# Performance work log

Hardware: AMD Instinct MI355X
Metric: run time of the kernel (lower is better)

## Reference

```python
import jax, jax.numpy as jnp
import numpy as np

N_NODES = 50000
N_EDGES = 800000
D = 64
D_OUT = 64


def setup_inputs() -> dict:
    key = jax.random.key(0)
    ks = jax.random.split(key, 7)
    h_src = jax.random.normal(ks[0], (N_NODES, D), dtype=jnp.float32)
    h_dst = jax.random.normal(ks[1], (N_NODES, D), dtype=jnp.float32)
    e = jax.random.normal(ks[2], (N_EDGES, D), dtype=jnp.float32)
    src = jax.random.randint(ks[3], (N_EDGES,), 0, N_NODES, dtype=jnp.int32)
    dst = jax.random.randint(ks[4], (N_EDGES,), 0, N_NODES, dtype=jnp.int32)
    W = jax.random.normal(ks[5], (D_OUT, 2 * D), dtype=jnp.float32) * 0.05  # nn.Linear weight [out, in]
    b = jax.random.normal(ks[6], (D_OUT,), dtype=jnp.float32) * 0.05
    return {"h_src": h_src, "h_dst": h_dst, "e": e, "src": src, "dst": dst, "W": W, "b": b}


def reference(h_src, h_dst, e, src, dst, W, b):
    # u_dot_e: per-edge dot product between gathered src features and edge features
    h_u = h_src[src]                                   # [E, D] gather
    score = jnp.sum(h_u * e, axis=-1)                  # [E]
    exp_s = jnp.exp(score)                             # raw exp, as in original (no max-subtract)
    # segment-sum exp over dst nodes, then edge-wise normalize (edge softmax)
    denom = jax.ops.segment_sum(exp_s, dst, num_segments=N_NODES)  # [N]
    pi = exp_s / denom[dst]                            # [E]
    # weighted neighbor aggregation: sum_e pi * h_src[src] into dst
    msg = h_u * pi[:, None]                            # [E, D]
    h_sum = jax.ops.segment_sum(msg, dst, num_segments=N_NODES)    # [N, D]
    # concat self features with aggregated neighbors, then linear
    h_total = jnp.concatenate([h_dst, h_sum], axis=1)  # [N, 2D]
    return h_total @ W.T + b                           # [N, D_OUT]
```

## Files before the change

### kernel.cpp

```cpp
#include <hip/hip_runtime.h>

#define N_NODES 50000
#define N_EDGES 800000
#define D 64
#define CAP 64

typedef float vf4 __attribute__((ext_vector_type(4)));

__global__ __launch_bounds__(256) void k1_bucket(
    const int* __restrict__ src, const int* __restrict__ dst,
    int* __restrict__ count, int2* __restrict__ slots) {
    int i = blockIdx.x * 256 + threadIdx.x;
    int s = src[i];
    int d = dst[i];
    int pos = atomicAdd(&count[d], 1);
    if (pos < CAP)
        slots[(size_t)d * CAP + pos] = make_int2(s, i);
}

__global__ __launch_bounds__(256, 4) void k2_agg(
    const vf4* __restrict__ h_src4, const vf4* __restrict__ e4,
    const int* __restrict__ count, const int2* __restrict__ slots,
    vf4* __restrict__ h_sum4) {
    int t = threadIdx.x;
    int node = blockIdx.x * 16 + (t >> 4);
    int l16 = t & 15;
    int cnt = count[node];
    cnt = cnt < CAP ? cnt : CAP;
    const int2* row = slots + (size_t)node * CAP;
    vf4 acc = {0.f, 0.f, 0.f, 0.f};
    float dsum = 0.f;
    int2 se = make_int2(0, 0);
    if (l16 < 8 && l16 < cnt) se = row[l16];
    for (int base = 0; base < cnt; base += 8) {
        int2 se_cur = se;
        int nxt = base + 8;
        se = make_int2(0, 0);
        if (l16 < 8 && nxt + l16 < cnt) se = row[nxt + l16];
        vf4 us[8], evs[8];
        #pragma unroll
        for (int j = 0; j < 8; ++j) {
            int sj = __shfl(se_cur.x, j, 16);
            int ej = __shfl(se_cur.y, j, 16);
            us[j]  = h_src4[(size_t)sj * 16 + l16];
            evs[j] = e4[(size_t)ej * 16 + l16];
        }
        #pragma unroll
        for (int j = 0; j < 8; ++j) {
            vf4 u = us[j], ev = evs[j];
            float p = u[0]*ev[0] + u[1]*ev[1] + u[2]*ev[2] + u[3]*ev[3];
            p += __shfl_xor(p, 1, 16);
            p += __shfl_xor(p, 2, 16);
            p += __shfl_xor(p, 4, 16);
            p += __shfl_xor(p, 8, 16);
            float w = __expf(p);
            w = (base + j < cnt) ? w : 0.f;
            acc += w * u;
            dsum += w;
        }
    }
    float inv = (cnt > 0) ? 1.f / dsum : 0.f;
    acc *= inv;
    h_sum4[(size_t)node * 16 + l16] = acc;
}

__global__ __launch_bounds__(256) void k3_linear(
    const vf4* __restrict__ h_dst4, const vf4* __restrict__ h_sum4,
    const float* __restrict__ W, const float* __restrict__ b,
    float* __restrict__ out) {
    __shared__ float Wl[128 * 65];
    __shared__ __align__(16) float ht[16][132];
    int t = threadIdx.x;
    for (int i = t; i < 128 * 64; i += 256) {
        int o = i >> 7, k = i & 127;
        Wl[k * 65 + o] = W[i];
    }
    int node0 = blockIdx.x * 16;
    {
        int n = t >> 4;
        int l16 = t & 15;
        int node = node0 + n;
        vf4 hd = h_dst4[(size_t)node * 16 + l16];
        vf4 hs = h_sum4[(size_t)node * 16 + l16];
        *(vf4*)&ht[n][l16 * 4] = hd;
        *(vf4*)&ht[n][64 + l16 * 4] = hs;
    }
    __syncthreads();

    int o = t & 63;
    int g = t >> 6;
    float bias = b[o];
    float a0 = bias, a1 = bias, a2 = bias, a3 = bias;
    const float* h0 = &ht[g * 4 + 0][0];
    const float* h1 = &ht[g * 4 + 1][0];
    const float* h2 = &ht[g * 4 + 2][0];
    const float* h3 = &ht[g * 4 + 3][0];
    #pragma unroll
    for (int k = 0; k < 128; k += 4) {
        float w0 = Wl[(k + 0) * 65 + o];
        float w1 = Wl[(k + 1) * 65 + o];
        float w2 = Wl[(k + 2) * 65 + o];
        float w3 = Wl[(k + 3) * 65 + o];
        vf4 p0 = *(const vf4*)&h0[k];
        vf4 p1 = *(const vf4*)&h1[k];
        vf4 p2 = *(const vf4*)&h2[k];
        vf4 p3 = *(const vf4*)&h3[k];
        a0 += p0[0]*w0 + p0[1]*w1 + p0[2]*w2 + p0[3]*w3;
        a1 += p1[0]*w0 + p1[1]*w1 + p1[2]*w2 + p1[3]*w3;
        a2 += p2[0]*w0 + p2[1]*w1 + p2[2]*w2 + p2[3]*w3;
        a3 += p3[0]*w0 + p3[1]*w1 + p3[2]*w2 + p3[3]*w3;
    }
    out[(size_t)(node0 + g * 4 + 0) * 64 + o] = a0;
    out[(size_t)(node0 + g * 4 + 1) * 64 + o] = a1;
    out[(size_t)(node0 + g * 4 + 2) * 64 + o] = a2;
    out[(size_t)(node0 + g * 4 + 3) * 64 + o] = a3;
}

extern "C" void kernel_launch(void* const* d_in, const int* in_sizes, int n_in,
                              void* d_out, int out_size, void* d_ws, size_t ws_size,
                              hipStream_t stream) {
    const float* h_src = (const float*)d_in[0];
    const float* h_dst = (const float*)d_in[1];
    const float* e     = (const float*)d_in[2];
    const int*   src   = (const int*)d_in[3];
    const int*   dst   = (const int*)d_in[4];
    const float* W     = (const float*)d_in[5];
    const float* b     = (const float*)d_in[6];
    float* out = (float*)d_out;

    auto align256 = [](size_t x) { return (x + 255) & ~(size_t)255; };
    char* ws = (char*)d_ws;
    int*  count = (int*)ws;
    int2* slots = (int2*)(ws + align256((size_t)N_NODES * 4));
    float* h_sum = (float*)(ws + align256((size_t)N_NODES * 4)
                               + align256((size_t)N_NODES * CAP * 8));

    hipMemsetAsync(count, 0, (size_t)N_NODES * 4, stream);

    k1_bucket<<<N_EDGES / 256, 256, 0, stream>>>(src, dst, count, slots);
    k2_agg<<<N_NODES / 16, 256, 0, stream>>>(
        (const vf4*)h_src, (const vf4*)e, count, slots, (vf4*)h_sum);
    k3_linear<<<(N_NODES + 15) / 16, 256, 0, stream>>>(
        (const vf4*)h_dst, (const vf4*)h_sum, W, b, out);
}
```

Before: 397.8 us.

## Compute edge exp-scores during bucketing and gather only source rows in aggregation

The per-edge dot product and exp now run inside the bucketing kernel. Each thread reads its edge's feature row in edge order and stores the exp weight in the slot in place of the edge index. The aggregation kernel then gathers only h_src rows, with no shuffle reduction. It also processes 16 slots per batch and allows higher occupancy. The trade-off is that h_src is now gathered twice, and the per-thread row reads in the bucketing kernel are strided and uncoalesced.

After: 443.3 us. 11.4% more time.

```diff
diff --git a/kernel.cpp b/kernel.cpp
--- a/kernel.cpp
+++ b/kernel.cpp
@@ -7,19 +7,30 @@
 
 typedef float vf4 __attribute__((ext_vector_type(4)));
 
-__global__ __launch_bounds__(256) void k1_bucket(
+__global__ __launch_bounds__(256) void k1_score_bucket(
+    const vf4* __restrict__ h_src4, const vf4* __restrict__ e4,
     const int* __restrict__ src, const int* __restrict__ dst,
     int* __restrict__ count, int2* __restrict__ slots) {
     int i = blockIdx.x * 256 + threadIdx.x;
     int s = src[i];
     int d = dst[i];
+    const vf4* u  = h_src4 + (size_t)s * 16;
+    const vf4* ev = e4 + (size_t)i * 16;
+    vf4 dacc = {0.f, 0.f, 0.f, 0.f};
+    #pragma unroll
+    for (int k = 0; k < 16; ++k) {
+        vf4 a = u[k];
+        vf4 bb = ev[k];
+        dacc += a * bb;
+    }
+    float w = __expf(dacc[0] + dacc[1] + dacc[2] + dacc[3]);
     int pos = atomicAdd(&count[d], 1);
     if (pos < CAP)
-        slots[(size_t)d * CAP + pos] = make_int2(s, i);
+        slots[(size_t)d * CAP + pos] = make_int2(s, __float_as_int(w));
 }
 
-__global__ __launch_bounds__(256, 4) void k2_agg(
-    const vf4* __restrict__ h_src4, const vf4* __restrict__ e4,
+__global__ __launch_bounds__(256, 6) void k2_agg(
+    const vf4* __restrict__ h_src4,
     const int* __restrict__ count, const int2* __restrict__ slots,
     vf4* __restrict__ h_sum4) {
     int t = threadIdx.x;
@@ -31,32 +42,19 @@
     vf4 acc = {0.f, 0.f, 0.f, 0.f};
     float dsum = 0.f;
     int2 se = make_int2(0, 0);
-    if (l16 < 8 && l16 < cnt) se = row[l16];
-    for (int base = 0; base < cnt; base += 8) {
-        int2 se_cur = se;
-        int nxt = base + 8;
+    if (l16 < cnt) se = row[l16];
+    for (int base = 0; base < cnt; base += 16) {
+        int2 cur = se;
+        int nxt = base + 16;
         se = make_int2(0, 0);
-        if (l16 < 8 && nxt + l16 < cnt) se = row[nxt + l16];
-        vf4 us[8], evs[8];
+        if (nxt + l16 < cnt) se = row[nxt + l16];
         #pragma unroll
-        for (int j = 0; j < 8; ++j) {
-            int sj = __shfl(se_cur.x, j, 16);
-            int ej = __shfl(se_cur.y, j, 16);
-            us[j]  = h_src4[(size_t)sj * 16 + l16];
-            evs[j] = e4[(size_t)ej * 16 + l16];
-        }
-        #pragma unroll
-        for (int j = 0; j < 8; ++j) {
-            vf4 u = us[j], ev = evs[j];
-            float p = u[0]*ev[0] + u[1]*ev[1] + u[2]*ev[2] + u[3]*ev[3];
-            p += __shfl_xor(p, 1, 16);
-            p += __shfl_xor(p, 2, 16);
-            p += __shfl_xor(p, 4, 16);
-            p += __shfl_xor(p, 8, 16);
-            float w = __expf(p);
-            w = (base + j < cnt) ? w : 0.f;
-            acc += w * u;
-            dsum += w;
+        for (int j = 0; j < 16; ++j) {
+            int sj = __shfl(cur.x, j, 16);
+            float wj = __int_as_float(__shfl(cur.y, j, 16));
+            vf4 u = h_src4[(size_t)sj * 16 + l16];
+            acc += wj * u;
+            dsum += wj;
         }
     }
     float inv = (cnt > 0) ? 1.f / dsum : 0.f;
@@ -137,9 +135,10 @@
 
     hipMemsetAsync(count, 0, (size_t)N_NODES * 4, stream);
 
-    k1_bucket<<<N_EDGES / 256, 256, 0, stream>>>(src, dst, count, slots);
+    k1_score_bucket<<<N_EDGES / 256, 256, 0, stream>>>(
+        (const vf4*)h_src, (const vf4*)e, src, dst, count, slots);
     k2_agg<<<N_NODES / 16, 256, 0, stream>>>(
-        (const vf4*)h_src, (const vf4*)e, count, slots, (vf4*)h_sum);
+        (const vf4*)h_src, count, slots, (vf4*)h_sum);
     k3_linear<<<(N_NODES + 15) / 16, 256, 0, stream>>>(
         (const vf4*)h_dst, (const vf4*)h_sum, W, b, out);
 }
```
